# Optimization experiments

Measured on AMD Instinct MI355X. Metric: run time of the kernel, lower is better.

## Reference

```python
import jax, jax.numpy as jnp
import numpy as np

STATE_DIM = 128
ACT_DIM = 32
ENC_K = 10   # encoder_spine_dim
DEC_K = 10   # decoder_dim
H0, H1 = 2048, 2048
BATCH = 16384
MAX_ACTION = 1.0
STD0 = 0.3872983346207417  # sqrt(0.15)


def setup_inputs() -> dict:
    key = jax.random.key(0)
    ks = jax.random.split(key, 10)
    state = jax.random.normal(ks[0], (BATCH, STATE_DIM), dtype=jnp.float32)
    # encoder params: mean linspace over mean_range, std constant
    mean_enc = jnp.broadcast_to(jnp.linspace(-3.0, 3.0, ENC_K, dtype=jnp.float32),
                                (1, STATE_DIM, ENC_K))
    std_enc = jnp.full((1, STATE_DIM, ENC_K), STD0, dtype=jnp.float32)
    def lin(k, fan_in, fan_out):
        bound = 1.0 / np.sqrt(fan_in)
        k1, k2 = jax.random.split(k)
        W = jax.random.uniform(k1, (fan_out, fan_in), jnp.float32, -bound, bound)
        b = jax.random.uniform(k2, (fan_out,), jnp.float32, -bound, bound)
        return W, b
    W1, b1 = lin(ks[1], STATE_DIM * ENC_K, H0)
    W2, b2 = lin(ks[2], H0, H1)
    W3, b3 = lin(ks[3], H1, ACT_DIM * DEC_K)
    # grouped conv1d: weight [act_dim, 1, dec_k], bias [act_dim]
    bound = 1.0 / np.sqrt(DEC_K)
    Wd = jax.random.uniform(ks[4], (ACT_DIM, 1, DEC_K), jnp.float32, -bound, bound)
    bd = jax.random.uniform(ks[5], (ACT_DIM,), jnp.float32, -bound, bound)
    return {"state": state, "mean_enc": mean_enc, "std_enc": std_enc,
            "W1": W1, "b1": b1, "W2": W2, "b2": b2, "W3": W3, "b3": b3,
            "Wd": Wd, "bd": bd}


def reference(state, mean_enc, std_enc, W1, b1, W2, b2, W3, b3, Wd, bd):
    # Population-coding encoder: sigmoid((obs - mean)/std), flattened
    spine = jax.nn.sigmoid((state[:, :, None] - mean_enc) / std_enc)  # [B, D, K]
    spine = spine.reshape(state.shape[0], -1)                         # [B, D*K]
    a = jax.nn.relu(spine @ W1.T + b1)
    a = jax.nn.relu(a @ W2.T + b2)
    a = a @ W3.T + b3                                                 # [B, A*Kd]
    d = a.reshape(-1, ACT_DIM, DEC_K)                                 # [B, A, Kd]
    # grouped Conv1d with kernel == length => per-channel dot product
    raw = jnp.einsum('bak,ak->ba', d, Wd[:, 0, :]) + bd               # [B, A]
    return MAX_ACTION * jnp.tanh(raw)
```

## Files before the change

kernel.cpp:

```cpp
#include <hip/hip_runtime.h>
#include <hip/hip_bf16.h>
#include <stdint.h>

#define BATCH   16384
#define SDIM    128
#define ENCK    10
#define ADIM    32
#define DECK    10
#define HID     2048
#define KSPINE  1280

typedef __bf16 bf16x8 __attribute__((ext_vector_type(8)));
typedef float  f32x4  __attribute__((ext_vector_type(4)));

typedef __attribute__((address_space(1))) const void kGlobalVoid;
typedef __attribute__((address_space(3))) void       kLdsVoid;

__device__ __forceinline__ unsigned short f2b(float f) {
  union { float f; unsigned u; } v; v.f = f;
  unsigned r = v.u + 0x7fffu + ((v.u >> 16) & 1u);
  return (unsigned short)(r >> 16);
}

__global__ void f2b_kernel(const float* __restrict__ in, unsigned* __restrict__ out, int n2) {
  int i = blockIdx.x * blockDim.x + threadIdx.x;
  if (i >= n2) return;
  float2 v = reinterpret_cast<const float2*>(in)[i];
  out[i] = (unsigned)f2b(v.x) | ((unsigned)f2b(v.y) << 16);
}

__global__ void encoder_kernel(const float* __restrict__ state,
                               const float* __restrict__ mean,
                               const float* __restrict__ stdv,
                               unsigned* __restrict__ spine) {
  int idx = blockIdx.x * blockDim.x + threadIdx.x;
  if (idx >= BATCH * SDIM) return;
  int d = idx & (SDIM - 1);
  float x = state[idx];
  float vals[ENCK];
#pragma unroll
  for (int k = 0; k < ENCK; ++k) {
    float z = (x - mean[d * ENCK + k]) / stdv[d * ENCK + k];
    vals[k] = 1.f / (1.f + __expf(-z));
  }
  unsigned* dst = spine + idx * (ENCK / 2);
#pragma unroll
  for (int k = 0; k < ENCK / 2; ++k)
    dst[k] = (unsigned)f2b(vals[2 * k]) | ((unsigned)f2b(vals[2 * k + 1]) << 16);
}

__global__ void weff_kernel(const float* __restrict__ W3, const float* __restrict__ Wd,
                            unsigned short* __restrict__ Weff) {
  int idx = blockIdx.x * 256 + threadIdx.x;
  int a = idx >> 11, j = idx & 2047;
  float s = 0.f;
#pragma unroll
  for (int k = 0; k < DECK; ++k)
    s += Wd[a * DECK + k] * W3[(size_t)(a * DECK + k) * HID + j];
  Weff[idx] = f2b(s);
}

__global__ void beff_kernel(const float* __restrict__ b3, const float* __restrict__ Wd,
                            const float* __restrict__ bd, float* __restrict__ beff) {
  int a = threadIdx.x;
  if (a >= ADIM) return;
  float s = bd[a];
#pragma unroll
  for (int k = 0; k < DECK; ++k) s += Wd[a * DECK + k] * b3[a * DECK + k];
  beff[a] = s;
}


#define A0B 0
#define B0B 32768
#define A1B 65536
#define B1B 98304

#define FENCE asm volatile("" ::: "memory")

#define STAGE(BASEPTR, R0A, R0B, LDS0, LDS1, KT)                                             \
  __builtin_amdgcn_global_load_lds((kGlobalVoid*)((BASEPTR) + (size_t)((R0A) + rs) * K + (KT) + ce), \
                                   (kLdsVoid*)(smem + (LDS0) + t * 16), 16, 0, 0);           \
  __builtin_amdgcn_global_load_lds((kGlobalVoid*)((BASEPTR) + (size_t)((R0B) + rs) * K + (KT) + ce), \
                                   (kLdsVoid*)(smem + (LDS1) + t * 16), 16, 0, 0);

#define DS_AF(DST, ABASE, MPN)                                                               \
  _Pragma("unroll")                                                                          \
  for (int j2 = 0; j2 < 2; ++j2) {                                                           \
    _Pragma("unroll")                                                                        \
    for (int ks = 0; ks < 2; ++ks) {                                                         \
      int rowl = wr * 128 + (MPN) * 32 + j2 * 16 + lr;                                       \
      DST[j2][ks] = *reinterpret_cast<const bf16x8*>(                                        \
          smem + (ABASE) + rowl * 128 + ((((ks) << 6) | (kh << 4)) ^ swz));                  \
    }                                                                                        \
  }

#define DS_BF(DST, BBASE)                                                                    \
  _Pragma("unroll")                                                                          \
  for (int n = 0; n < 4; ++n) {                                                              \
    _Pragma("unroll")                                                                        \
    for (int ks = 0; ks < 2; ++ks) {                                                         \
      int rowl = wc * 64 + n * 16 + lr;                                                      \
      DST[n][ks] = *reinterpret_cast<const bf16x8*>(                                         \
          smem + (BBASE) + rowl * 128 + ((((ks) << 6) | (kh << 4)) ^ swz));                  \
    }                                                                                        \
  }

#define MFMA16(MP, AF, BF)                                                                   \
  _Pragma("unroll")                                                                          \
  for (int j2 = 0; j2 < 2; ++j2)                                                             \
    _Pragma("unroll")                                                                        \
    for (int n = 0; n < 4; ++n)                                                              \
      _Pragma("unroll")                                                                      \
      for (int ks = 0; ks < 2; ++ks)                                                         \
        acc[(MP) * 2 + j2][n] = __builtin_amdgcn_mfma_f32_16x16x32_bf16(                     \
            AF[j2][ks], BF[n][ks], acc[(MP) * 2 + j2][n], 0, 0, 0);

#define PH(MP, AF_CUR, AF_NXT, BF_CUR, NXT_ABASE, NXT_MP, DOVM, DOB, NXT_BF, NXT_BBASE, STG) \
  do {                                                                                       \
    asm volatile("s_waitcnt lgkmcnt(0)" ::: "memory");                                       \
    __builtin_amdgcn_sched_barrier(0);                                                       \
    if (DOVM) {                                                                              \
      asm volatile("s_waitcnt vmcnt(6)" ::: "memory");                                       \
      __builtin_amdgcn_sched_barrier(0);                                                     \
    }                                                                                        \
    __builtin_amdgcn_s_setprio(1);                                                           \
    MFMA16(MP, AF_CUR, BF_CUR);                                                              \
    __builtin_amdgcn_s_setprio(0);                                                           \
    DS_AF(AF_NXT, NXT_ABASE, NXT_MP);                                                        \
    if (DOB) { DS_BF(NXT_BF, NXT_BBASE); }                                                   \
    STG;                                                                                     \
    FENCE;                                                                                   \
    __builtin_amdgcn_s_barrier();                                                            \
  } while (0)

__global__ __launch_bounds__(512, 2) void gemm256(
    const unsigned short* __restrict__ A,
    const unsigned short* __restrict__ Bw,
    const float* __restrict__ bias,
    unsigned short* __restrict__ Cout,
    int K, int NI) {
  __shared__ char smem[131072];

  const int t    = threadIdx.x;
  const int lane = t & 63;
  const int w    = t >> 6;
  const int wr   = w >> 2;
  const int wc   = w & 3;
  const int lr   = lane & 15;
  const int kh   = lane >> 4;
  const int swz  = (lr & 7) << 4;
  const int rs   = t >> 3;
  const int ce   = ((t & 7) ^ (rs & 7)) << 3;

  const int bid = blockIdx.x;
  const int xcd = bid & 7, idx = bid >> 3;
  const int row0 = (xcd * 8 + (idx >> 3)) * 256;
  const int col0 = (idx & 7) * 256;

  f32x4 acc[8][4];
#pragma unroll
  for (int m = 0; m < 8; ++m)
#pragma unroll
    for (int n = 0; n < 4; ++n)
      acc[m][n] = (f32x4){0.f, 0.f, 0.f, 0.f};

  bf16x8 af0[2][2], af1[2][2], bfv0[4][2], bfv1[4][2];

  STAGE(Bw, col0 + 0,   col0 + 64,  B0B + 0,     B0B + 8192,  0);
  STAGE(Bw, col0 + 128, col0 + 192, B0B + 16384, B0B + 24576, 0);
  STAGE(A,  row0 + 0,   row0 + 128, A0B + 0,     A0B + 16384, 0);
  STAGE(A,  row0 + 64,  row0 + 192, A0B + 8192,  A0B + 24576, 0);
  STAGE(Bw, col0 + 0,   col0 + 64,  B1B + 0,     B1B + 8192,  64);
  STAGE(Bw, col0 + 128, col0 + 192, B1B + 16384, B1B + 24576, 64);
  STAGE(A,  row0 + 0,   row0 + 128, A1B + 0,     A1B + 16384, 64);
  asm volatile("s_waitcnt vmcnt(6)" ::: "memory");
  FENCE;
  __builtin_amdgcn_s_barrier();
  DS_AF(af0, A0B, 0);
  DS_BF(bfv0, B0B);

  for (int i = 0; i < NI; ++i) {
    int kt0 = i << 7;
    int kt1 = kt0 + 64;
    int kt2 = kt0 + 128; if (kt2 >= K) kt2 -= K;
    int kt3 = kt0 + 192; if (kt3 >= K) kt3 -= K;

    PH(0, af0, af1, bfv0, A0B, 1, false, false, bfv1, B1B,
       STAGE(A,  row0 + 64,  row0 + 192, A1B + 8192,  A1B + 24576, kt1));
    PH(1, af1, af0, bfv0, A0B, 2, false, false, bfv1, B1B,
       STAGE(Bw, col0 + 0,   col0 + 64,  B0B + 0,     B0B + 8192,  kt2));
    PH(2, af0, af1, bfv0, A0B, 3, false, false, bfv1, B1B,
       STAGE(Bw, col0 + 128, col0 + 192, B0B + 16384, B0B + 24576, kt2));
    PH(3, af1, af0, bfv0, A1B, 0, true,  true,  bfv1, B1B,
       STAGE(A,  row0 + 0,   row0 + 128, A0B + 0,     A0B + 16384, kt2));
    PH(0, af0, af1, bfv1, A1B, 1, false, false, bfv0, B0B,
       STAGE(A,  row0 + 64,  row0 + 192, A0B + 8192,  A0B + 24576, kt2));
    PH(1, af1, af0, bfv1, A1B, 2, false, false, bfv0, B0B,
       STAGE(Bw, col0 + 0,   col0 + 64,  B1B + 0,     B1B + 8192,  kt3));
    PH(2, af0, af1, bfv1, A1B, 3, false, false, bfv0, B0B,
       STAGE(Bw, col0 + 128, col0 + 192, B1B + 16384, B1B + 24576, kt3));
    PH(3, af1, af0, bfv1, A0B, 0, true,  true,  bfv0, B0B,
       STAGE(A,  row0 + 0,   row0 + 128, A1B + 0,     A1B + 16384, kt3));
  }

#pragma unroll
  for (int m = 0; m < 8; ++m) {
    int gr0 = row0 + wr * 128 + m * 16 + kh * 4;
#pragma unroll
    for (int n = 0; n < 4; ++n) {
      int gc = col0 + wc * 64 + n * 16 + lr;
      float bv = bias[gc];
#pragma unroll
      for (int v = 0; v < 4; ++v) {
        float val = fmaxf(acc[m][n][v] + bv, 0.f);
        Cout[(size_t)(gr0 + v) * 2048 + gc] = f2b(val);
      }
    }
  }
}

__global__ __launch_bounds__(128) void gemm_skinny(
    const unsigned short* __restrict__ A,
    const unsigned short* __restrict__ Bw,
    const float* __restrict__ beff,
    float* __restrict__ out) {
  const int t = threadIdx.x, lane = t & 63, w = t >> 6;
  const int lr = lane & 15, kh = lane >> 4;
  const int row0 = (blockIdx.x * 2 + w) * 16;
  f32x4 acc[2];
  acc[0] = (f32x4){0.f, 0.f, 0.f, 0.f};
  acc[1] = (f32x4){0.f, 0.f, 0.f, 0.f};

  const unsigned short* Arow = A  + (size_t)(row0 + lr) * HID + kh * 8;
  const unsigned short* B0   = Bw + (size_t)(lr) * HID + kh * 8;
  const unsigned short* B1   = Bw + (size_t)(16 + lr) * HID + kh * 8;

#pragma unroll 4
  for (int kt = 0; kt < HID; kt += 32) {
    bf16x8 a  = *reinterpret_cast<const bf16x8*>(Arow + kt);
    bf16x8 b0 = *reinterpret_cast<const bf16x8*>(B0 + kt);
    bf16x8 b1 = *reinterpret_cast<const bf16x8*>(B1 + kt);
    acc[0] = __builtin_amdgcn_mfma_f32_16x16x32_bf16(a, b0, acc[0], 0, 0, 0);
    acc[1] = __builtin_amdgcn_mfma_f32_16x16x32_bf16(a, b1, acc[1], 0, 0, 0);
  }
#pragma unroll
  for (int n = 0; n < 2; ++n)
#pragma unroll
    for (int v = 0; v < 4; ++v) {
      int row = row0 + kh * 4 + v;
      int col = n * 16 + lr;
      out[(size_t)row * ADIM + col] = tanhf(acc[n][v] + beff[col]);
    }
}

extern "C" void kernel_launch(void* const* d_in, const int* in_sizes, int n_in,
                              void* d_out, int out_size, void* d_ws, size_t ws_size,
                              hipStream_t stream) {
  const float* state    = (const float*)d_in[0];
  const float* mean_enc = (const float*)d_in[1];
  const float* std_enc  = (const float*)d_in[2];
  const float* W1 = (const float*)d_in[3];
  const float* b1 = (const float*)d_in[4];
  const float* W2 = (const float*)d_in[5];
  const float* b2 = (const float*)d_in[6];
  const float* W3 = (const float*)d_in[7];
  const float* b3 = (const float*)d_in[8];
  const float* Wd = (const float*)d_in[9];
  const float* bd = (const float*)d_in[10];

  char* ws = (char*)d_ws;
  unsigned short* W1b   = (unsigned short*)(ws + 0);
  unsigned short* W2b   = (unsigned short*)(ws + 5242880);
  unsigned short* Weff  = (unsigned short*)(ws + 13631488);
  float*          beff  = (float*)(ws + 13762560);
  unsigned short* spine = (unsigned short*)(ws + 13762688);
  unsigned short* h1    = (unsigned short*)(ws + 55705728);
  unsigned short* h2    = (unsigned short*)(ws + 122814592);

  f2b_kernel<<<5120, 256, 0, stream>>>(W1, (unsigned*)W1b, 1310720);
  f2b_kernel<<<8192, 256, 0, stream>>>(W2, (unsigned*)W2b, 2097152);
  weff_kernel<<<256, 256, 0, stream>>>(W3, Wd, Weff);
  beff_kernel<<<1, 64, 0, stream>>>(b3, Wd, bd, beff);

  encoder_kernel<<<(BATCH * SDIM) / 256, 256, 0, stream>>>(state, mean_enc, std_enc, (unsigned*)spine);

  gemm256<<<512, 512, 0, stream>>>(spine, W1b, b1, h1, KSPINE, KSPINE / 128);
  gemm256<<<512, 512, 0, stream>>>(h1,    W2b, b2, h2, HID,    HID / 128);
  gemm_skinny<<<BATCH / 32, 128, 0, stream>>>(h2, Weff, beff, (float*)d_out);
}
```

Baseline: 249.3 us.

## Switch GEMM to 4 waves with 128x128 per-wave tiles and coarser phases

The 256x256 block GEMM now runs with 256 threads (4 waves in a 2x2 grid), each wave computing a 128x128 sub-tile with 64 accumulators. That halves the LDS fragment reads per MFMA. The pipeline changes from eight fine-grained phases to four larger ones, each doing 64 MFMAs, then loading the next fragments and staging a whole 256-row slab. In exchange the kernel uses far more registers (256 accumulator floats plus fragments), occupancy drops to one block of 4 waves per CU, and each phase now waits on vmcnt(0), which may expose memory latency.

```diff
diff --git a/kernel.cpp b/kernel.cpp
--- a/kernel.cpp
+++ b/kernel.cpp
@@ -78,63 +78,56 @@
 
 #define FENCE asm volatile("" ::: "memory")
 
-#define STAGE(BASEPTR, R0A, R0B, LDS0, LDS1, KT)                                             \
-  __builtin_amdgcn_global_load_lds((kGlobalVoid*)((BASEPTR) + (size_t)((R0A) + rs) * K + (KT) + ce), \
-                                   (kLdsVoid*)(smem + (LDS0) + t * 16), 16, 0, 0);           \
-  __builtin_amdgcn_global_load_lds((kGlobalVoid*)((BASEPTR) + (size_t)((R0B) + rs) * K + (KT) + ce), \
-                                   (kLdsVoid*)(smem + (LDS1) + t * 16), 16, 0, 0);
-
-#define DS_AF(DST, ABASE, MPN)                                                               \
-  _Pragma("unroll")                                                                          \
-  for (int j2 = 0; j2 < 2; ++j2) {                                                           \
+#define STAGE8(BASEPTR, R0, LDSB, KT)                                                        \
+  _Pragma("unroll")                                                                          \
+  for (int g = 0; g < 8; ++g) {                                                              \
+    __builtin_amdgcn_global_load_lds(                                                        \
+        (kGlobalVoid*)((BASEPTR) + (size_t)((R0) + g * 32 + rs) * K + (KT) + ce),            \
+        (kLdsVoid*)(smem + (LDSB) + g * 4096 + t * 16), 16, 0, 0);                           \
+  }
+
+#define DS_AF8(DST, ABASE, KS)                                                               \
+  _Pragma("unroll")                                                                          \
+  for (int m = 0; m < 8; ++m) {                                                              \
+    int rowl = wr * 128 + m * 16 + lr;                                                       \
+    DST[m] = *reinterpret_cast<const bf16x8*>(                                               \
+        smem + (ABASE) + rowl * 128 + ((((KS) << 6) | (kh << 4)) ^ swz));                    \
+  }
+
+#define DS_BF8(DST, BBASE, KS)                                                               \
+  _Pragma("unroll")                                                                          \
+  for (int n = 0; n < 8; ++n) {                                                              \
+    int rowl = wc * 128 + n * 16 + lr;                                                       \
+    DST[n] = *reinterpret_cast<const bf16x8*>(                                               \
+        smem + (BBASE) + rowl * 128 + ((((KS) << 6) | (kh << 4)) ^ swz));                    \
+  }
+
+#define MFMA64(AF, BF)                                                                       \
+  _Pragma("unroll")                                                                          \
+  for (int m = 0; m < 8; ++m)                                                                \
     _Pragma("unroll")                                                                        \
-    for (int ks = 0; ks < 2; ++ks) {                                                         \
-      int rowl = wr * 128 + (MPN) * 32 + j2 * 16 + lr;                                       \
-      DST[j2][ks] = *reinterpret_cast<const bf16x8*>(                                        \
-          smem + (ABASE) + rowl * 128 + ((((ks) << 6) | (kh << 4)) ^ swz));                  \
-    }                                                                                        \
-  }
-
-#define DS_BF(DST, BBASE)                                                                    \
-  _Pragma("unroll")                                                                          \
-  for (int n = 0; n < 4; ++n) {                                                              \
-    _Pragma("unroll")                                                                        \
-    for (int ks = 0; ks < 2; ++ks) {                                                         \
-      int rowl = wc * 64 + n * 16 + lr;                                                      \
-      DST[n][ks] = *reinterpret_cast<const bf16x8*>(                                         \
-          smem + (BBASE) + rowl * 128 + ((((ks) << 6) | (kh << 4)) ^ swz));                  \
-    }                                                                                        \
-  }
-
-#define MFMA16(MP, AF, BF)                                                                   \
-  _Pragma("unroll")                                                                          \
-  for (int j2 = 0; j2 < 2; ++j2)                                                             \
-    _Pragma("unroll")                                                                        \
-    for (int n = 0; n < 4; ++n)                                                              \
-      _Pragma("unroll")                                                                      \
-      for (int ks = 0; ks < 2; ++ks)                                                         \
-        acc[(MP) * 2 + j2][n] = __builtin_amdgcn_mfma_f32_16x16x32_bf16(                     \
-            AF[j2][ks], BF[n][ks], acc[(MP) * 2 + j2][n], 0, 0, 0);
-
-#define PH(MP, AF_CUR, AF_NXT, BF_CUR, NXT_ABASE, NXT_MP, DOVM, DOB, NXT_BF, NXT_BBASE, STG) \
+    for (int n = 0; n < 8; ++n)                                                              \
+      acc[m][n] = __builtin_amdgcn_mfma_f32_16x16x32_bf16(AF[m], BF[n], acc[m][n], 0, 0, 0);
+
+#define PH4(AF_C, BF_C, AF_N, BF_N, SH_A, SH_B, SH_KS, DOVM, STG)                            \
   do {                                                                                       \
     asm volatile("s_waitcnt lgkmcnt(0)" ::: "memory");                                       \
     __builtin_amdgcn_sched_barrier(0);                                                       \
+    __builtin_amdgcn_s_setprio(1);                                                           \
+    MFMA64(AF_C, BF_C);                                                                      \
+    __builtin_amdgcn_s_setprio(0);                                                           \
     if (DOVM) {                                                                              \
-      asm volatile("s_waitcnt vmcnt(6)" ::: "memory");                                       \
+      asm volatile("s_waitcnt vmcnt(0)" ::: "memory");                                       \
       __builtin_amdgcn_sched_barrier(0);                                                     \
     }                                                                                        \
-    __builtin_amdgcn_s_setprio(1);                                                           \
-    MFMA16(MP, AF_CUR, BF_CUR);                                                              \
-    __builtin_amdgcn_s_setprio(0);                                                           \
-    DS_AF(AF_NXT, NXT_ABASE, NXT_MP);                                                        \
-    if (DOB) { DS_BF(NXT_BF, NXT_BBASE); }                                                   \
+    DS_AF8(AF_N, SH_A, SH_KS);                                                               \
+    DS_BF8(BF_N, SH_B, SH_KS);                                                               \
     STG;                                                                                     \
     FENCE;                                                                                   \
     __builtin_amdgcn_s_barrier();                                                            \
   } while (0)
 
-__global__ __launch_bounds__(512, 2) void gemm256(
+__global__ __launch_bounds__(256, 1) void gemm256(
     const unsigned short* __restrict__ A,
     const unsigned short* __restrict__ Bw,
     const float* __restrict__ bias,
@@ -145,8 +138,8 @@
   const int t    = threadIdx.x;
   const int lane = t & 63;
   const int w    = t >> 6;
-  const int wr   = w >> 2;
-  const int wc   = w & 3;
+  const int wr   = w >> 1;
+  const int wc   = w & 1;
   const int lr   = lane & 15;
   const int kh   = lane >> 4;
   const int swz  = (lr & 7) << 4;
@@ -158,27 +151,23 @@
   const int row0 = (xcd * 8 + (idx >> 3)) * 256;
   const int col0 = (idx & 7) * 256;
 
-  f32x4 acc[8][4];
+  f32x4 acc[8][8];
 #pragma unroll
   for (int m = 0; m < 8; ++m)
 #pragma unroll
-    for (int n = 0; n < 4; ++n)
+    for (int n = 0; n < 8; ++n)
       acc[m][n] = (f32x4){0.f, 0.f, 0.f, 0.f};
 
-  bf16x8 af0[2][2], af1[2][2], bfv0[4][2], bfv1[4][2];
-
-  STAGE(Bw, col0 + 0,   col0 + 64,  B0B + 0,     B0B + 8192,  0);
-  STAGE(Bw, col0 + 128, col0 + 192, B0B + 16384, B0B + 24576, 0);
-  STAGE(A,  row0 + 0,   row0 + 128, A0B + 0,     A0B + 16384, 0);
-  STAGE(A,  row0 + 64,  row0 + 192, A0B + 8192,  A0B + 24576, 0);
-  STAGE(Bw, col0 + 0,   col0 + 64,  B1B + 0,     B1B + 8192,  64);
-  STAGE(Bw, col0 + 128, col0 + 192, B1B + 16384, B1B + 24576, 64);
-  STAGE(A,  row0 + 0,   row0 + 128, A1B + 0,     A1B + 16384, 64);
-  asm volatile("s_waitcnt vmcnt(6)" ::: "memory");
+  bf16x8 afc[8], afn[8], bfc[8], bfn[8];
+
+  STAGE8(A,  row0, A0B, 0);
+  STAGE8(Bw, col0, B0B, 0);
+  STAGE8(A,  row0, A1B, 64);
+  asm volatile("s_waitcnt vmcnt(8)" ::: "memory");
   FENCE;
   __builtin_amdgcn_s_barrier();
-  DS_AF(af0, A0B, 0);
-  DS_BF(bfv0, B0B);
+  DS_AF8(afc, A0B, 0);
+  DS_BF8(bfc, B0B, 0);
 
   for (int i = 0; i < NI; ++i) {
     int kt0 = i << 7;
@@ -186,30 +175,18 @@
     int kt2 = kt0 + 128; if (kt2 >= K) kt2 -= K;
     int kt3 = kt0 + 192; if (kt3 >= K) kt3 -= K;
 
-    PH(0, af0, af1, bfv0, A0B, 1, false, false, bfv1, B1B,
-       STAGE(A,  row0 + 64,  row0 + 192, A1B + 8192,  A1B + 24576, kt1));
-    PH(1, af1, af0, bfv0, A0B, 2, false, false, bfv1, B1B,
-       STAGE(Bw, col0 + 0,   col0 + 64,  B0B + 0,     B0B + 8192,  kt2));
-    PH(2, af0, af1, bfv0, A0B, 3, false, false, bfv1, B1B,
-       STAGE(Bw, col0 + 128, col0 + 192, B0B + 16384, B0B + 24576, kt2));
-    PH(3, af1, af0, bfv0, A1B, 0, true,  true,  bfv1, B1B,
-       STAGE(A,  row0 + 0,   row0 + 128, A0B + 0,     A0B + 16384, kt2));
-    PH(0, af0, af1, bfv1, A1B, 1, false, false, bfv0, B0B,
-       STAGE(A,  row0 + 64,  row0 + 192, A0B + 8192,  A0B + 24576, kt2));
-    PH(1, af1, af0, bfv1, A1B, 2, false, false, bfv0, B0B,
-       STAGE(Bw, col0 + 0,   col0 + 64,  B1B + 0,     B1B + 8192,  kt3));
-    PH(2, af0, af1, bfv1, A1B, 3, false, false, bfv0, B0B,
-       STAGE(Bw, col0 + 128, col0 + 192, B1B + 16384, B1B + 24576, kt3));
-    PH(3, af1, af0, bfv1, A0B, 0, true,  true,  bfv0, B0B,
-       STAGE(A,  row0 + 0,   row0 + 128, A1B + 0,     A1B + 16384, kt3));
+    PH4(afc, bfc, afn, bfn, A0B, B0B, 1, false, STAGE8(Bw, col0, B1B, kt1));
+    PH4(afn, bfn, afc, bfc, A1B, B1B, 0, true,  STAGE8(A,  row0, A0B, kt2));
+    PH4(afc, bfc, afn, bfn, A1B, B1B, 1, false, STAGE8(Bw, col0, B0B, kt2));
+    PH4(afn, bfn, afc, bfc, A0B, B0B, 0, true,  STAGE8(A,  row0, A1B, kt3));
   }
 
 #pragma unroll
   for (int m = 0; m < 8; ++m) {
     int gr0 = row0 + wr * 128 + m * 16 + kh * 4;
 #pragma unroll
-    for (int n = 0; n < 4; ++n) {
-      int gc = col0 + wc * 64 + n * 16 + lr;
+    for (int n = 0; n < 8; ++n) {
+      int gc = col0 + wc * 128 + n * 16 + lr;
       float bv = bias[gc];
 #pragma unroll
       for (int v = 0; v < 4; ++v) {
@@ -285,7 +262,7 @@
 
   encoder_kernel<<<(BATCH * SDIM) / 256, 256, 0, stream>>>(state, mean_enc, std_enc, (unsigned*)spine);
 
-  gemm256<<<512, 512, 0, stream>>>(spine, W1b, b1, h1, KSPINE, KSPINE / 128);
-  gemm256<<<512, 512, 0, stream>>>(h1,    W2b, b2, h2, HID,    HID / 128);
+  gemm256<<<512, 256, 0, stream>>>(spine, W1b, b1, h1, KSPINE, KSPINE / 128);
+  gemm256<<<512, 256, 0, stream>>>(h1,    W2b, b2, h2, HID,    HID / 128);
   gemm_skinny<<<BATCH / 32, 128, 0, stream>>>(h2, Weff, beff, (float*)d_out);
 }
```

After: 457.9 us. 1.84x slower.

## Load B fragments directly from global into registers, halve LDS footprint

Applied to the files above, without the earlier changes.

The GEMM stops staging the weight (B) tile through LDS. Each wave now loads its B fragments straight from global memory into registers one k-step ahead, and only A is staged through a double-buffered LDS region of 64KB. The pipeline is reorganized into a prefetch phase plus plain phases with adjusted vmcnt waits. This removes the LDS write/read traffic for B and the LDS pressure. In exchange, B global loads are duplicated across the two wave rows, use uncoalesced per-lane row reads, and register pressure goes up.

```diff
diff --git a/kernel.cpp b/kernel.cpp
--- a/kernel.cpp
+++ b/kernel.cpp
@@ -72,17 +72,26 @@
 
 
 #define A0B 0
-#define B0B 32768
-#define A1B 65536
-#define B1B 98304
+#define A1B 32768
 
 #define FENCE asm volatile("" ::: "memory")
 
-#define STAGE(BASEPTR, R0A, R0B, LDS0, LDS1, KT)                                             \
-  __builtin_amdgcn_global_load_lds((kGlobalVoid*)((BASEPTR) + (size_t)((R0A) + rs) * K + (KT) + ce), \
-                                   (kLdsVoid*)(smem + (LDS0) + t * 16), 16, 0, 0);           \
-  __builtin_amdgcn_global_load_lds((kGlobalVoid*)((BASEPTR) + (size_t)((R0B) + rs) * K + (KT) + ce), \
-                                   (kLdsVoid*)(smem + (LDS1) + t * 16), 16, 0, 0);
+#define STAGE4(R0, LDSB, KT)                                                                 \
+  _Pragma("unroll")                                                                          \
+  for (int g = 0; g < 4; ++g) {                                                              \
+    __builtin_amdgcn_global_load_lds(                                                        \
+        (kGlobalVoid*)(A + (size_t)((R0) + g * 64 + rs) * K + (KT) + ce),                    \
+        (kLdsVoid*)(smem + (LDSB) + g * 8192 + t * 16), 16, 0, 0);                           \
+  }
+
+#define GLB_BF(DST, KT)                                                                      \
+  _Pragma("unroll")                                                                          \
+  for (int n = 0; n < 4; ++n) {                                                              \
+    _Pragma("unroll")                                                                        \
+    for (int ks = 0; ks < 2; ++ks) {                                                         \
+      DST[n][ks] = *reinterpret_cast<const bf16x8*>(Bbase + (size_t)n * 16 * K + (KT) + ks * 32); \
+    }                                                                                        \
+  }
 
 #define DS_AF(DST, ABASE, MPN)                                                               \
   _Pragma("unroll")                                                                          \
@@ -95,17 +104,6 @@
     }                                                                                        \
   }
 
-#define DS_BF(DST, BBASE)                                                                    \
-  _Pragma("unroll")                                                                          \
-  for (int n = 0; n < 4; ++n) {                                                              \
-    _Pragma("unroll")                                                                        \
-    for (int ks = 0; ks < 2; ++ks) {                                                         \
-      int rowl = wc * 64 + n * 16 + lr;                                                      \
-      DST[n][ks] = *reinterpret_cast<const bf16x8*>(                                         \
-          smem + (BBASE) + rowl * 128 + ((((ks) << 6) | (kh << 4)) ^ swz));                  \
-    }                                                                                        \
-  }
-
 #define MFMA16(MP, AF, BF)                                                                   \
   _Pragma("unroll")                                                                          \
   for (int j2 = 0; j2 < 2; ++j2)                                                             \
@@ -116,20 +114,33 @@
         acc[(MP) * 2 + j2][n] = __builtin_amdgcn_mfma_f32_16x16x32_bf16(                     \
             AF[j2][ks], BF[n][ks], acc[(MP) * 2 + j2][n], 0, 0, 0);
 
-#define PH(MP, AF_CUR, AF_NXT, BF_CUR, NXT_ABASE, NXT_MP, DOVM, DOB, NXT_BF, NXT_BBASE, STG) \
+#define PH_P0(AF_C, AF_N, BF_C, BF_N, CURB, NXTB, KTN)                                       \
   do {                                                                                       \
     asm volatile("s_waitcnt lgkmcnt(0)" ::: "memory");                                       \
     __builtin_amdgcn_sched_barrier(0);                                                       \
+    STAGE4(row0, NXTB, KTN);                                                                 \
+    GLB_BF(BF_N, KTN);                                                                       \
+    FENCE;                                                                                   \
+    __builtin_amdgcn_s_setprio(1);                                                           \
+    MFMA16(0, AF_C, BF_C);                                                                   \
+    __builtin_amdgcn_s_setprio(0);                                                           \
+    DS_AF(AF_N, CURB, 1);                                                                    \
+    FENCE;                                                                                   \
+    __builtin_amdgcn_s_barrier();                                                            \
+  } while (0)
+
+#define PH_PLAIN(MP, AF_C, AF_N, BF_C, RDB, RD_MP, DOVM)                                     \
+  do {                                                                                       \
+    asm volatile("s_waitcnt lgkmcnt(0)" ::: "memory");                                       \
+    __builtin_amdgcn_sched_barrier(0);                                                       \
+    __builtin_amdgcn_s_setprio(1);                                                           \
+    MFMA16(MP, AF_C, BF_C);                                                                  \
+    __builtin_amdgcn_s_setprio(0);                                                           \
     if (DOVM) {                                                                              \
-      asm volatile("s_waitcnt vmcnt(6)" ::: "memory");                                       \
+      asm volatile("s_waitcnt vmcnt(8)" ::: "memory");                                       \
       __builtin_amdgcn_sched_barrier(0);                                                     \
     }                                                                                        \
-    __builtin_amdgcn_s_setprio(1);                                                           \
-    MFMA16(MP, AF_CUR, BF_CUR);                                                              \
-    __builtin_amdgcn_s_setprio(0);                                                           \
-    DS_AF(AF_NXT, NXT_ABASE, NXT_MP);                                                        \
-    if (DOB) { DS_BF(NXT_BF, NXT_BBASE); }                                                   \
-    STG;                                                                                     \
+    DS_AF(AF_N, RDB, RD_MP);                                                                 \
     FENCE;                                                                                   \
     __builtin_amdgcn_s_barrier();                                                            \
   } while (0)
@@ -140,7 +151,7 @@
     const float* __restrict__ bias,
     unsigned short* __restrict__ Cout,
     int K, int NI) {
-  __shared__ char smem[131072];
+  __shared__ char smem[65536];
 
   const int t    = threadIdx.x;
   const int lane = t & 63;
@@ -158,6 +169,8 @@
   const int row0 = (xcd * 8 + (idx >> 3)) * 256;
   const int col0 = (idx & 7) * 256;
 
+  const unsigned short* Bbase = Bw + (size_t)(col0 + wc * 64 + lr) * K + kh * 8;
+
   f32x4 acc[8][4];
 #pragma unroll
   for (int m = 0; m < 8; ++m)
@@ -165,43 +178,28 @@
     for (int n = 0; n < 4; ++n)
       acc[m][n] = (f32x4){0.f, 0.f, 0.f, 0.f};
 
-  bf16x8 af0[2][2], af1[2][2], bfv0[4][2], bfv1[4][2];
-
-  STAGE(Bw, col0 + 0,   col0 + 64,  B0B + 0,     B0B + 8192,  0);
-  STAGE(Bw, col0 + 128, col0 + 192, B0B + 16384, B0B + 24576, 0);
-  STAGE(A,  row0 + 0,   row0 + 128, A0B + 0,     A0B + 16384, 0);
-  STAGE(A,  row0 + 64,  row0 + 192, A0B + 8192,  A0B + 24576, 0);
-  STAGE(Bw, col0 + 0,   col0 + 64,  B1B + 0,     B1B + 8192,  64);
-  STAGE(Bw, col0 + 128, col0 + 192, B1B + 16384, B1B + 24576, 64);
-  STAGE(A,  row0 + 0,   row0 + 128, A1B + 0,     A1B + 16384, 64);
-  asm volatile("s_waitcnt vmcnt(6)" ::: "memory");
+  bf16x8 afc[2][2], afn[2][2], bfc[4][2], bfn[4][2];
+
+  STAGE4(row0, A0B, 0);
+  GLB_BF(bfc, 0);
+  asm volatile("s_waitcnt vmcnt(8)" ::: "memory");
   FENCE;
   __builtin_amdgcn_s_barrier();
-  DS_AF(af0, A0B, 0);
-  DS_BF(bfv0, B0B);
+  DS_AF(afc, A0B, 0);
 
   for (int i = 0; i < NI; ++i) {
     int kt0 = i << 7;
     int kt1 = kt0 + 64;
-    int kt2 = kt0 + 128; if (kt2 >= K) kt2 -= K;
-    int kt3 = kt0 + 192; if (kt3 >= K) kt3 -= K;
-
-    PH(0, af0, af1, bfv0, A0B, 1, false, false, bfv1, B1B,
-       STAGE(A,  row0 + 64,  row0 + 192, A1B + 8192,  A1B + 24576, kt1));
-    PH(1, af1, af0, bfv0, A0B, 2, false, false, bfv1, B1B,
-       STAGE(Bw, col0 + 0,   col0 + 64,  B0B + 0,     B0B + 8192,  kt2));
-    PH(2, af0, af1, bfv0, A0B, 3, false, false, bfv1, B1B,
-       STAGE(Bw, col0 + 128, col0 + 192, B0B + 16384, B0B + 24576, kt2));
-    PH(3, af1, af0, bfv0, A1B, 0, true,  true,  bfv1, B1B,
-       STAGE(A,  row0 + 0,   row0 + 128, A0B + 0,     A0B + 16384, kt2));
-    PH(0, af0, af1, bfv1, A1B, 1, false, false, bfv0, B0B,
-       STAGE(A,  row0 + 64,  row0 + 192, A0B + 8192,  A0B + 24576, kt2));
-    PH(1, af1, af0, bfv1, A1B, 2, false, false, bfv0, B0B,
-       STAGE(Bw, col0 + 0,   col0 + 64,  B1B + 0,     B1B + 8192,  kt3));
-    PH(2, af0, af1, bfv1, A1B, 3, false, false, bfv0, B0B,
-       STAGE(Bw, col0 + 128, col0 + 192, B1B + 16384, B1B + 24576, kt3));
-    PH(3, af1, af0, bfv1, A0B, 0, true,  true,  bfv0, B0B,
-       STAGE(A,  row0 + 0,   row0 + 128, A1B + 0,     A1B + 16384, kt3));
+    int kt2 = kt0 + 128; if (kt2 >= K) kt2 = 0;
+
+    PH_P0 (   afc, afn, bfc, bfn, A0B, A1B, kt1);
+    PH_PLAIN(1, afn, afc, bfc, A0B, 2, false);
+    PH_PLAIN(2, afc, afn, bfc, A0B, 3, true);
+    PH_PLAIN(3, afn, afc, bfc, A1B, 0, false);
+    PH_P0 (   afc, afn, bfn, bfc, A1B, A0B, kt2);
+    PH_PLAIN(1, afn, afc, bfn, A1B, 2, false);
+    PH_PLAIN(2, afc, afn, bfn, A1B, 3, true);
+    PH_PLAIN(3, afn, afc, bfn, A0B, 0, false);
   }
 
 #pragma unroll
```

Result: slower. 380.2 us (+52.5%).

## Spread B-fragment LDS reads across phases and interleave with MFMAs via sched groups

Applied to the files above, without the earlier changes.

Instead of loading all next B fragments in the last phase of each half-iteration, each phase now reads one quarter of the next B buffer. Sched_group_barrier patterns interleave MFMA, DS reads and VMEM issues within a phase to overlap LDS latency with matrix math. The vmcnt waits are reshuffled (vmcnt(2) in phase 0, vmcnt(6) in phase 3), and the prologue now waits for all loads. This risks wrong synchronization, because B1B is read from phase 0 while its later stages may still be in flight, and it adds register pressure from holding two full B fragment sets.

```diff
diff --git a/kernel.cpp b/kernel.cpp
--- a/kernel.cpp
+++ b/kernel.cpp
@@ -95,6 +95,14 @@
     }                                                                                        \
   }
 
+#define DS_B2(DST, NP, BBASE)                                                                \
+  _Pragma("unroll")                                                                          \
+  for (int ks = 0; ks < 2; ++ks) {                                                           \
+    int rowl = wc * 64 + (NP) * 16 + lr;                                                     \
+    DST[NP][ks] = *reinterpret_cast<const bf16x8*>(                                          \
+        smem + (BBASE) + rowl * 128 + ((((ks) << 6) | (kh << 4)) ^ swz));                    \
+  }
+
 #define DS_BF(DST, BBASE)                                                                    \
   _Pragma("unroll")                                                                          \
   for (int n = 0; n < 4; ++n) {                                                              \
@@ -116,20 +124,37 @@
         acc[(MP) * 2 + j2][n] = __builtin_amdgcn_mfma_f32_16x16x32_bf16(                     \
             AF[j2][ks], BF[n][ks], acc[(MP) * 2 + j2][n], 0, 0, 0);
 
-#define PH(MP, AF_CUR, AF_NXT, BF_CUR, NXT_ABASE, NXT_MP, DOVM, DOB, NXT_BF, NXT_BBASE, STG) \
+#define SGB_PHASE                                                                            \
+  __builtin_amdgcn_sched_group_barrier(0x8, 2, 0);                                           \
+  __builtin_amdgcn_sched_group_barrier(0x100, 1, 0);                                         \
+  __builtin_amdgcn_sched_group_barrier(0x8, 2, 0);                                           \
+  __builtin_amdgcn_sched_group_barrier(0x100, 1, 0);                                         \
+  __builtin_amdgcn_sched_group_barrier(0x20, 2, 0);                                          \
+  __builtin_amdgcn_sched_group_barrier(0x8, 3, 0);                                           \
+  __builtin_amdgcn_sched_group_barrier(0x100, 1, 0);                                         \
+  __builtin_amdgcn_sched_group_barrier(0x8, 3, 0);                                           \
+  __builtin_amdgcn_sched_group_barrier(0x100, 1, 0);                                         \
+  __builtin_amdgcn_sched_group_barrier(0x8, 3, 0);                                           \
+  __builtin_amdgcn_sched_group_barrier(0x100, 1, 0);                                         \
+  __builtin_amdgcn_sched_group_barrier(0x8, 3, 0);                                           \
+  __builtin_amdgcn_sched_group_barrier(0x100, 1, 0);
+
+#define VM_NONE
+#define VM2 asm volatile("s_waitcnt vmcnt(2)" ::: "memory"); __builtin_amdgcn_sched_barrier(0);
+#define VM6 asm volatile("s_waitcnt vmcnt(6)" ::: "memory"); __builtin_amdgcn_sched_barrier(0);
+
+#define PH(MP, AF_C, AF_N, BF_C, BF_N, NXT_A, NXT_MP, BBASE_N, VMW, STG)                     \
   do {                                                                                       \
     asm volatile("s_waitcnt lgkmcnt(0)" ::: "memory");                                       \
     __builtin_amdgcn_sched_barrier(0);                                                       \
-    if (DOVM) {                                                                              \
-      asm volatile("s_waitcnt vmcnt(6)" ::: "memory");                                       \
-      __builtin_amdgcn_sched_barrier(0);                                                     \
-    }                                                                                        \
+    VMW                                                                                      \
     __builtin_amdgcn_s_setprio(1);                                                           \
-    MFMA16(MP, AF_CUR, BF_CUR);                                                              \
+    MFMA16(MP, AF_C, BF_C);                                                                  \
     __builtin_amdgcn_s_setprio(0);                                                           \
-    DS_AF(AF_NXT, NXT_ABASE, NXT_MP);                                                        \
-    if (DOB) { DS_BF(NXT_BF, NXT_BBASE); }                                                   \
+    DS_AF(AF_N, NXT_A, NXT_MP);                                                              \
+    DS_B2(BF_N, MP, BBASE_N);                                                                \
     STG;                                                                                     \
+    SGB_PHASE;                                                                               \
     FENCE;                                                                                   \
     __builtin_amdgcn_s_barrier();                                                            \
   } while (0)
@@ -165,7 +190,7 @@
     for (int n = 0; n < 4; ++n)
       acc[m][n] = (f32x4){0.f, 0.f, 0.f, 0.f};
 
-  bf16x8 af0[2][2], af1[2][2], bfv0[4][2], bfv1[4][2];
+  bf16x8 afc[2][2], afn[2][2], bfA[4][2], bfB[4][2];
 
   STAGE(Bw, col0 + 0,   col0 + 64,  B0B + 0,     B0B + 8192,  0);
   STAGE(Bw, col0 + 128, col0 + 192, B0B + 16384, B0B + 24576, 0);
@@ -174,11 +199,11 @@
   STAGE(Bw, col0 + 0,   col0 + 64,  B1B + 0,     B1B + 8192,  64);
   STAGE(Bw, col0 + 128, col0 + 192, B1B + 16384, B1B + 24576, 64);
   STAGE(A,  row0 + 0,   row0 + 128, A1B + 0,     A1B + 16384, 64);
-  asm volatile("s_waitcnt vmcnt(6)" ::: "memory");
+  asm volatile("s_waitcnt vmcnt(0)" ::: "memory");
   FENCE;
   __builtin_amdgcn_s_barrier();
-  DS_AF(af0, A0B, 0);
-  DS_BF(bfv0, B0B);
+  DS_AF(afc, A0B, 0);
+  DS_BF(bfA, B0B);
 
   for (int i = 0; i < NI; ++i) {
     int kt0 = i << 7;
@@ -186,21 +211,21 @@
     int kt2 = kt0 + 128; if (kt2 >= K) kt2 -= K;
     int kt3 = kt0 + 192; if (kt3 >= K) kt3 -= K;
 
-    PH(0, af0, af1, bfv0, A0B, 1, false, false, bfv1, B1B,
+    PH(0, afc, afn, bfA, bfB, A0B, 1, B1B, VM2,
        STAGE(A,  row0 + 64,  row0 + 192, A1B + 8192,  A1B + 24576, kt1));
-    PH(1, af1, af0, bfv0, A0B, 2, false, false, bfv1, B1B,
+    PH(1, afn, afc, bfA, bfB, A0B, 2, B1B, VM_NONE,
        STAGE(Bw, col0 + 0,   col0 + 64,  B0B + 0,     B0B + 8192,  kt2));
-    PH(2, af0, af1, bfv0, A0B, 3, false, false, bfv1, B1B,
+    PH(2, afc, afn, bfA, bfB, A0B, 3, B1B, VM_NONE,
        STAGE(Bw, col0 + 128, col0 + 192, B0B + 16384, B0B + 24576, kt2));
-    PH(3, af1, af0, bfv0, A1B, 0, true,  true,  bfv1, B1B,
+    PH(3, afn, afc, bfA, bfB, A1B, 0, B1B, VM6,
        STAGE(A,  row0 + 0,   row0 + 128, A0B + 0,     A0B + 16384, kt2));
-    PH(0, af0, af1, bfv1, A1B, 1, false, false, bfv0, B0B,
+    PH(0, afc, afn, bfB, bfA, A1B, 1, B0B, VM2,
        STAGE(A,  row0 + 64,  row0 + 192, A0B + 8192,  A0B + 24576, kt2));
-    PH(1, af1, af0, bfv1, A1B, 2, false, false, bfv0, B0B,
+    PH(1, afn, afc, bfB, bfA, A1B, 2, B0B, VM_NONE,
        STAGE(Bw, col0 + 0,   col0 + 64,  B1B + 0,     B1B + 8192,  kt3));
-    PH(2, af0, af1, bfv1, A1B, 3, false, false, bfv0, B0B,
+    PH(2, afc, afn, bfB, bfA, A1B, 3, B0B, VM_NONE,
        STAGE(Bw, col0 + 128, col0 + 192, B1B + 16384, B1B + 24576, kt3));
-    PH(3, af1, af0, bfv1, A0B, 0, true,  true,  bfv0, B0B,
+    PH(3, afn, afc, bfB, bfA, A0B, 0, B0B, VM6,
        STAGE(A,  row0 + 0,   row0 + 128, A1B + 0,     A1B + 16384, kt3));
   }
 
```

Measured after the change: 249.1 us. About the same (-0.1%).
